# Performance work log

Hardware: AMD Instinct MI355X
Metric: run time of the kernel (lower is better)

The kernel has to match this reference:

```python
import jax, jax.numpy as jnp
import numpy as np

EMBED_DIM = 1024
NUM_HEADS = 16
HEAD_DIM = EMBED_DIM // NUM_HEADS
# Source divides by scale = head_dim**-0.5, i.e. multiplies logits by sqrt(head_dim).
INV_SCALE = float(HEAD_DIM) ** 0.5


def setup_inputs() -> dict:
    key = jax.random.key(0)
    ks = jax.random.split(key, 9)
    E = EMBED_DIM
    s = 1.0 / np.sqrt(E)
    x = jax.random.normal(ks[0], (2, 2048, E), dtype=jnp.float32)
    Wq = jax.random.uniform(ks[1], (E, E), jnp.float32, -s, s)
    bq = jax.random.uniform(ks[2], (E,), jnp.float32, -s, s)
    Wk = jax.random.uniform(ks[3], (E, E), jnp.float32, -s, s)
    bk = jax.random.uniform(ks[4], (E,), jnp.float32, -s, s)
    Wv = jax.random.uniform(ks[5], (E, E), jnp.float32, -s, s)
    bv = jax.random.uniform(ks[6], (E,), jnp.float32, -s, s)
    Wo = jax.random.uniform(ks[7], (E, E), jnp.float32, -s, s)
    bo = jax.random.uniform(ks[8], (E,), jnp.float32, -s, s)
    return {"x": x, "Wq": Wq, "bq": bq, "Wk": Wk, "bk": bk,
            "Wv": Wv, "bv": bv, "Wo": Wo, "bo": bo}


def reference(x, Wq, bq, Wk, bk, Wv, bv, Wo, bo):
    B, N, C = x.shape
    H, D = NUM_HEADS, HEAD_DIM
    # nn.Linear: y = x @ W.T + b
    q = (x @ Wq.T + bq).reshape(B, N, H, D).transpose(0, 2, 1, 3)  # [B,H,N,D]
    k = (x @ Wk.T + bk).reshape(B, N, H, D).transpose(0, 2, 1, 3)
    v = (x @ Wv.T + bv).reshape(B, N, H, D).transpose(0, 2, 1, 3)
    # Faithful to source: logits = QK^T / (head_dim**-0.5) = QK^T * sqrt(head_dim)
    logits = jnp.einsum('bhnd,bhmd->bhnm', q, k) * INV_SCALE  # [B,H,N,N]
    attn = jax.nn.softmax(logits, axis=-1)
    h = jnp.einsum('bhnm,bhmd->bhnd', attn, v)  # [B,H,N,D]
    concat_h = h.transpose(0, 2, 1, 3).reshape(B, N, C)
    return concat_h @ Wo.T + bo
```

## Files before the change

kernel.cpp:

```cpp
#include <hip/hip_runtime.h>
#include <math.h>

#define B_ 2
#define N_ 2048
#define E_ 1024
#define H_ 16
#define D_ 64

typedef unsigned short US;
typedef _Float16 h16x8 __attribute__((ext_vector_type(8)));
typedef _Float16 h16x4 __attribute__((ext_vector_type(4)));
typedef __fp16 fp16x2 __attribute__((ext_vector_type(2)));
typedef float f32x4 __attribute__((ext_vector_type(4)));
#define MFMA16F(a,b,c)  __builtin_amdgcn_mfma_f32_16x16x32_f16(a,b,c,0,0,0)
#define MFMA161(a,b,c)  __builtin_amdgcn_mfma_f32_16x16x16f16(a,b,c,0,0,0)
#define SCL  11.5415603828f

union HU { _Float16 h; US u; };
__device__ __forceinline__ US f2h(float f){ HU x; x.h = (_Float16)f; return x.u; }
__device__ __forceinline__ unsigned pkrtz(float a, float b){
  union { fp16x2 h; unsigned u; } x;
  x.h = __builtin_amdgcn_cvt_pkrtz(a, b);
  return x.u;
}

union U8 { US u[8]; uint4 v; };
union U4 { US u[4]; uint2 v; };
union UPA { unsigned u[2]; h16x4 h; };

__device__ __forceinline__ void glds16(const US* g, US* l){
  __builtin_amdgcn_global_load_lds(
    (const __attribute__((address_space(1))) unsigned int*)(const void*)g,
    (__attribute__((address_space(3))) unsigned int*)(void*)l, 16, 0, 0);
}

__global__ __launch_bounds__(256) void conv_all(
    const float* __restrict__ x,
    const float* __restrict__ w0, const float* __restrict__ w1,
    const float* __restrict__ w2, const float* __restrict__ w3,
    US* __restrict__ xh, US* __restrict__ Wall)
{
  const int id = blockIdx.x;
  const float* s; US* d; size_t off;
  if (id < 2048) { s = x; d = xh; off = (size_t)id*2048; }
  else {
    int j = id - 2048, wsel = j>>9;
    off = (size_t)(j&511)*2048;
    s = (wsel==0)?w0:(wsel==1)?w1:(wsel==2)?w2:w3;
    d = Wall + (size_t)wsel*1048576;
  }
  size_t i = off + (size_t)threadIdx.x*8;
  float f[8];
  *(float4*)&f[0] = *(const float4*)&s[i];
  *(float4*)&f[4] = *(const float4*)&s[i+4];
  U8 h;
  #pragma unroll
  for (int j=0;j<8;++j) h.u[j] = f2h(f[j]);
  *(uint4*)&d[i] = h.v;
}

__global__ __launch_bounds__(256,3) void qkv_gemm(
    const US* __restrict__ A, const US* __restrict__ Wall,
    const float* __restrict__ bq, const float* __restrict__ bk, const float* __restrict__ bv,
    US* __restrict__ Qf, US* __restrict__ Kf, US* __restrict__ Vtb)
{
  __shared__ __align__(16) US sA[128*32];
  __shared__ __align__(16) US sW[128*32];
  const int z = blockIdx.z;
  const US* W = Wall + (size_t)z*1048576;
  const float* bias = (z==0)?bq:(z==1)?bk:bv;

  const int t = threadIdx.x;
  const int w = t>>6, lane = t&63;
  const int q = lane>>4, c = lane&15;
  const int mq = (w>>1)*64, nq = (w&1)*64;
  const int gm0 = blockIdx.y*128, gn0 = blockIdx.x*128;
  const int r16 = lane>>2, seg = lane&3;

  f32x4 acc[4][4] = {};
  for (int kb = 0; kb < 1024; kb += 32) {
    #pragma unroll
    for (int p=0;p<2;++p){
      int rb = (w*2+p)*16;
      glds16(&A[(size_t)(gm0 + rb + r16)*1024 + kb + seg*8], &sA[rb*32]);
      glds16(&W[(size_t)(gn0 + rb + r16)*1024 + kb + seg*8], &sW[rb*32]);
    }
    __syncthreads();
    h16x8 af[4], wf[4];
    #pragma unroll
    for (int rt=0;rt<4;++rt) af[rt] = *(const h16x8*)&sA[(mq+rt*16+c)*32 + q*8];
    #pragma unroll
    for (int ct=0;ct<4;++ct) wf[ct] = *(const h16x8*)&sW[(nq+ct*16+c)*32 + q*8];
    #pragma unroll
    for (int rt=0;rt<4;++rt)
      #pragma unroll
      for (int ct=0;ct<4;++ct)
        acc[rt][ct] = MFMA16F(af[rt], wf[ct], acc[rt][ct]);
    __syncthreads();
  }
  #pragma unroll
  for (int rt=0;rt<4;++rt)
  #pragma unroll
  for (int ct=0;ct<4;++ct) {
    int col = gn0 + nq + ct*16 + c;
    float bv_ = bias[col];
    int rowb = gm0 + mq + rt*16 + q*4;
    int hh = col>>6, d = col & 63;
    if (z==2) {
      int b = rowb>>11, n = rowb & (N_-1);
      U4 pk;
      #pragma unroll
      for (int r=0;r<4;++r) pk.u[r] = f2h(acc[rt][ct][r] + bv_);
      *(uint2*)&Vtb[((size_t)(b*H_+hh)*D_ + d)*N_ + n] = pk.v;
    } else {
      US* dst = (z==0) ? Qf : Kf;
      #pragma unroll
      for (int r=0;r<4;++r) {
        int row = rowb + r;
        float v = acc[rt][ct][r] + bv_;
        if (z==0) v *= SCL;
        int b = row>>11, n = row & (N_-1);
        dst[((size_t)(b*H_+hh)*N_+n)*D_ + d] = f2h(v);
      }
    }
  }
}

__global__ __launch_bounds__(256,4) void o_gemm(
    const US* __restrict__ A, const US* __restrict__ W,
    const float* __restrict__ bias, float* __restrict__ out)
{
  __shared__ __align__(16) US sA[128*32];
  __shared__ __align__(16) US sW[64*32];
  const int t = threadIdx.x;
  const int w = t>>6, lane = t&63;
  const int q = lane>>4, c = lane&15;
  const int gm0 = blockIdx.y*128, gn0 = blockIdx.x*64;
  const int r16 = lane>>2, seg = lane&3;

  f32x4 acc[2][4] = {};
  for (int kb = 0; kb < 1024; kb += 32) {
    glds16(&A[(size_t)(gm0 + w*32      + r16)*1024 + kb + seg*8], &sA[(w*32)*32]);
    glds16(&A[(size_t)(gm0 + w*32 + 16 + r16)*1024 + kb + seg*8], &sA[(w*32+16)*32]);
    glds16(&W[(size_t)(gn0 + w*16      + r16)*1024 + kb + seg*8], &sW[(w*16)*32]);
    __syncthreads();
    h16x8 af0 = *(const h16x8*)&sA[(w*32+c)*32 + q*8];
    h16x8 af1 = *(const h16x8*)&sA[(w*32+16+c)*32 + q*8];
    #pragma unroll
    for (int ct=0; ct<4; ++ct){
      h16x8 wf = *(const h16x8*)&sW[(ct*16+c)*32 + q*8];
      acc[0][ct] = MFMA16F(af0, wf, acc[0][ct]);
      acc[1][ct] = MFMA16F(af1, wf, acc[1][ct]);
    }
    __syncthreads();
  }
  #pragma unroll
  for (int rt=0; rt<2; ++rt)
  #pragma unroll
  for (int ct=0; ct<4; ++ct) {
    int col = gn0 + ct*16 + c;
    float bv_ = bias[col];
    int rowb = gm0 + w*32 + rt*16 + q*4;
    #pragma unroll
    for (int r=0;r<4;++r)
      out[(size_t)(rowb+r)*1024 + col] = acc[rt][ct][r] + bv_;
  }
}

#define KSTR2 72
#define VSTR  136
__global__ __launch_bounds__(512,6) void attn(
    const US* __restrict__ Qf, const US* __restrict__ Kf, const US* __restrict__ Vt,
    US* __restrict__ Hout)
{
  __shared__ __align__(16) US sK [128*KSTR2];
  __shared__ __align__(16) US sVt[64*VSTR];
  const int t = threadIdx.x;
  const int w = t>>6, lane = t&63, q = lane>>4, c = lane&15;
  const int id = blockIdx.x;
  const int bh = ((id & 7) << 2) | ((id >> 3) & 3);
  const int n0 = (id >> 5) * 128;
  const US* Kp = Kf + (size_t)bh * (N_*D_);
  const US* Vp = Vt + (size_t)bh * (D_*N_);

  const size_t qoff = (size_t)bh*(N_*D_) + (size_t)(n0 + w*16 + c)*D_;
  h16x8 qb0 = *(const h16x8*)&Qf[qoff + q*8];
  h16x8 qb1 = *(const h16x8*)&Qf[qoff + 32 + q*8];
  h16x4 vones;
  #pragma unroll
  for (int j=0;j<4;++j) vones[j] = (_Float16)1.0f;

  float mi = -INFINITY;
  f32x4 o[5] = {};

  const int kr = t>>3, kc8 = (t&7)*8;
  const int vr = t>>4, vc8 = (t&15)*8;

  for (int mt=0; mt<16; ++mt) {
    const int m0 = mt*128;
    #pragma unroll
    for (int p=0;p<2;++p){
      int r = p*64 + kr;
      *(uint4*)&sK[r*KSTR2 + kc8] = *(const uint4*)&Kp[(size_t)(m0 + r)*D_ + kc8];
    }
    #pragma unroll
    for (int p=0;p<2;++p){
      int r = p*32 + vr;
      *(uint4*)&sVt[r*VSTR + vc8] = *(const uint4*)&Vp[(size_t)r*N_ + m0 + vc8];
    }
    __syncthreads();

    f32x4 s[8];
    __builtin_amdgcn_s_setprio(1);
    #pragma unroll
    for (int f=0; f<8; ++f){
      h16x8 k0 = *(const h16x8*)&sK[(f*16+c)*KSTR2 + q*8];
      h16x8 k1 = *(const h16x8*)&sK[(f*16+c)*KSTR2 + 32 + q*8];
      f32x4 sv = {};
      sv = MFMA16F(k0, qb0, sv);
      sv = MFMA16F(k1, qb1, sv);
      s[f] = sv;
    }
    __builtin_amdgcn_s_setprio(0);

    f32x4 vm = s[0];
    #pragma unroll
    for (int f=1; f<8; ++f){
      vm[0]=fmaxf(vm[0],s[f][0]); vm[1]=fmaxf(vm[1],s[f][1]);
      vm[2]=fmaxf(vm[2],s[f][2]); vm[3]=fmaxf(vm[3],s[f][3]);
    }
    float v = fmaxf(fmaxf(vm[0],vm[1]), fmaxf(vm[2],vm[3]));
    v = fmaxf(v, __shfl_xor(v, 16));
    v = fmaxf(v, __shfl_xor(v, 32));
    float mnew = fmaxf(mi, v);
    if (!__all(v <= mi)) {
      float alpha = exp2f(mi-mnew);
      float ar[4];
      #pragma unroll
      for (int r=0; r<4; ++r) ar[r] = __shfl(alpha, q*4+r);
      #pragma unroll
      for (int dt=0; dt<5; ++dt){
        o[dt][0]*=ar[0]; o[dt][1]*=ar[1]; o[dt][2]*=ar[2]; o[dt][3]*=ar[3];
      }
    }
    mi = mnew;
    #pragma unroll
    for (int f=0; f<8; ++f){
      float p0 = exp2f(s[f][0]-mnew);
      float p1 = exp2f(s[f][1]-mnew);
      float p2 = exp2f(s[f][2]-mnew);
      float p3 = exp2f(s[f][3]-mnew);
      UPA pa;
      pa.u[0] = pkrtz(p0, p1);
      pa.u[1] = pkrtz(p2, p3);
      h16x4 pah = pa.h;
      __builtin_amdgcn_s_setprio(1);
      #pragma unroll
      for (int dt=0; dt<4; ++dt){
        h16x4 vf = *(const h16x4*)&sVt[(dt*16+c)*VSTR + f*16 + q*4];
        o[dt] = MFMA161(pah, vf, o[dt]);
      }
      o[4] = MFMA161(pah, vones, o[4]);
      __builtin_amdgcn_s_setprio(0);
    }
    __syncthreads();
  }

  const int b = bh>>4, hh = bh&15;
  float ir[4];
  #pragma unroll
  for (int r=0; r<4; ++r) ir[r] = 1.0f / o[4][r];
  #pragma unroll
  for (int dt=0; dt<4; ++dt){
    #pragma unroll
    for (int r=0; r<4; ++r){
      int n = n0 + w*16 + q*4 + r;
      int d = dt*16 + c;
      Hout[((size_t)(b*N_+n)*H_+hh)*D_ + d] = f2h(o[dt][r] * ir[r]);
    }
  }
}

extern "C" void kernel_launch(void* const* d_in, const int* in_sizes, int n_in,
                              void* d_out, int out_size, void* d_ws, size_t ws_size,
                              hipStream_t stream)
{
  const float* x  = (const float*)d_in[0];
  const float* Wq = (const float*)d_in[1];
  const float* bq = (const float*)d_in[2];
  const float* Wk = (const float*)d_in[3];
  const float* bk = (const float*)d_in[4];
  const float* Wv = (const float*)d_in[5];
  const float* bv = (const float*)d_in[6];
  const float* Wo = (const float*)d_in[7];
  const float* bo = (const float*)d_in[8];
  US* ws  = (US*)d_ws;
  const size_t M1 = 1048576;
  US* xh   = ws;
  US* Wall = ws + 4*M1;
  US* Qf   = ws + 8*M1;
  US* Kf   = ws + 12*M1;
  US* Vtb  = ws + 16*M1;
  US* Hf   = ws + 20*M1;

  conv_all<<<4096, 256, 0, stream>>>(x, Wq, Wk, Wv, Wo, xh, Wall);
  qkv_gemm<<<dim3(8,32,3), 256, 0, stream>>>(xh, Wall, bq, bk, bv, Qf, Kf, Vtb);
  attn<<<512, 512, 0, stream>>>(Qf, Kf, Vtb, Hf);
  o_gemm<<<dim3(16,32), 256, 0, stream>>>(Hf, Wall + 3*M1, bo, (float*)d_out);
}
```

Before: 223.5 us.

## Double-buffer K/V tiles in attention with register prefetch of next tile

Makes the K and V shared-memory tiles double-buffered. The next tile's global loads are issued into registers before the QK^T and PV compute and written to the alternate buffer afterwards, so only one barrier per iteration remains. The goal is to hide global-memory latency behind MFMA work. In exchange, LDS use doubles, launch bounds drop from 6 to 4 blocks per CU, and the prefetch registers add register pressure.

```diff
diff --git a/kernel.cpp b/kernel.cpp
--- a/kernel.cpp
+++ b/kernel.cpp
@@ -169,12 +169,12 @@
 
 #define KSTR2 72
 #define VSTR  136
-__global__ __launch_bounds__(512,6) void attn(
+__global__ __launch_bounds__(512,4) void attn(
     const US* __restrict__ Qf, const US* __restrict__ Kf, const US* __restrict__ Vt,
     US* __restrict__ Hout)
 {
-  __shared__ __align__(16) US sK [128*KSTR2];
-  __shared__ __align__(16) US sVt[64*VSTR];
+  __shared__ __align__(16) US sK [2][128*KSTR2];
+  __shared__ __align__(16) US sVt[2][64*VSTR];
   const int t = threadIdx.x;
   const int w = t>>6, lane = t&63, q = lane>>4, c = lane&15;
   const int id = blockIdx.x;
@@ -196,26 +196,37 @@
   const int kr = t>>3, kc8 = (t&7)*8;
   const int vr = t>>4, vc8 = (t&15)*8;
 
+  #pragma unroll
+  for (int p=0;p<2;++p){
+    int r = p*64 + kr;
+    *(uint4*)&sK[0][r*KSTR2 + kc8] = *(const uint4*)&Kp[(size_t)r*D_ + kc8];
+  }
+  #pragma unroll
+  for (int p=0;p<2;++p){
+    int r = p*32 + vr;
+    *(uint4*)&sVt[0][r*VSTR + vc8] = *(const uint4*)&Vp[(size_t)r*N_ + vc8];
+  }
+  __syncthreads();
+
   for (int mt=0; mt<16; ++mt) {
-    const int m0 = mt*128;
-    #pragma unroll
-    for (int p=0;p<2;++p){
-      int r = p*64 + kr;
-      *(uint4*)&sK[r*KSTR2 + kc8] = *(const uint4*)&Kp[(size_t)(m0 + r)*D_ + kc8];
-    }
-    #pragma unroll
-    for (int p=0;p<2;++p){
-      int r = p*32 + vr;
-      *(uint4*)&sVt[r*VSTR + vc8] = *(const uint4*)&Vp[(size_t)r*N_ + m0 + vc8];
-    }
-    __syncthreads();
+    const int cur = mt&1;
+    uint4 kreg[2], vreg[2];
+    if (mt < 15){
+      const int m1 = (mt+1)*128;
+      #pragma unroll
+      for (int p=0;p<2;++p)
+        kreg[p] = *(const uint4*)&Kp[(size_t)(m1 + p*64 + kr)*D_ + kc8];
+      #pragma unroll
+      for (int p=0;p<2;++p)
+        vreg[p] = *(const uint4*)&Vp[(size_t)(p*32 + vr)*N_ + m1 + vc8];
+    }
 
     f32x4 s[8];
     __builtin_amdgcn_s_setprio(1);
     #pragma unroll
     for (int f=0; f<8; ++f){
-      h16x8 k0 = *(const h16x8*)&sK[(f*16+c)*KSTR2 + q*8];
-      h16x8 k1 = *(const h16x8*)&sK[(f*16+c)*KSTR2 + 32 + q*8];
+      h16x8 k0 = *(const h16x8*)&sK[cur][(f*16+c)*KSTR2 + q*8];
+      h16x8 k1 = *(const h16x8*)&sK[cur][(f*16+c)*KSTR2 + 32 + q*8];
       f32x4 sv = {};
       sv = MFMA16F(k0, qb0, sv);
       sv = MFMA16F(k1, qb1, sv);
@@ -257,11 +268,20 @@
       __builtin_amdgcn_s_setprio(1);
       #pragma unroll
       for (int dt=0; dt<4; ++dt){
-        h16x4 vf = *(const h16x4*)&sVt[(dt*16+c)*VSTR + f*16 + q*4];
+        h16x4 vf = *(const h16x4*)&sVt[cur][(dt*16+c)*VSTR + f*16 + q*4];
         o[dt] = MFMA161(pah, vf, o[dt]);
       }
       o[4] = MFMA161(pah, vones, o[4]);
       __builtin_amdgcn_s_setprio(0);
+    }
+
+    if (mt < 15){
+      #pragma unroll
+      for (int p=0;p<2;++p)
+        *(uint4*)&sK[cur^1][(p*64+kr)*KSTR2 + kc8] = kreg[p];
+      #pragma unroll
+      for (int p=0;p<2;++p)
+        *(uint4*)&sVt[cur^1][(p*32+vr)*VSTR + vc8] = vreg[p];
     }
     __syncthreads();
   }
```

Result: faster. 209.9 us (-6.1%).

## Double-buffer K/V tiles with direct global-to-LDS loads and software-pipelined QK

Applied to the files above, without the earlier changes.

Double-buffers the K and V^T tiles in shared memory and loads them with asynchronous global-to-LDS copies (glds16) into XOR-swizzled layouts instead of padded strides. The QK^T MFMAs for the next tile are issued alongside the PV MFMAs of the current tile, overlapping memory latency with compute. It also adds lazy max rescaling that only updates the running max when it grows by more than 8 in log2 space, and a tree-shaped max reduction. Shared memory use rises and the occupancy hint drops from 6 to 4 waves. The lazy rescale lets exponentials reach up to 2^8 before being rounded to fp16.

```diff
diff --git a/kernel.cpp b/kernel.cpp
--- a/kernel.cpp
+++ b/kernel.cpp
@@ -167,14 +167,12 @@
   }
 }
 
-#define KSTR2 72
-#define VSTR  136
-__global__ __launch_bounds__(512,6) void attn(
+__global__ __launch_bounds__(512,4) void attn(
     const US* __restrict__ Qf, const US* __restrict__ Kf, const US* __restrict__ Vt,
     US* __restrict__ Hout)
 {
-  __shared__ __align__(16) US sK [128*KSTR2];
-  __shared__ __align__(16) US sVt[64*VSTR];
+  __shared__ __align__(16) US sK [2][128*64];
+  __shared__ __align__(16) US sVt[2][64*128];
   const int t = threadIdx.x;
   const int w = t>>6, lane = t&63, q = lane>>4, c = lane&15;
   const int id = blockIdx.x;
@@ -193,48 +191,57 @@
   float mi = -INFINITY;
   f32x4 o[5] = {};
 
-  const int kr = t>>3, kc8 = (t&7)*8;
-  const int vr = t>>4, vc8 = (t&15)*8;
+  const int klr = lane>>3, klc = lane&7;
+  const int vlr = lane>>4, vlc = lane&15;
+
+  #define STAGE(MT, BUF)                                                              \
+    { const int m0_ = (MT)*128;                                                       \
+      _Pragma("unroll")                                                               \
+      for (int p=0;p<2;++p){                                                          \
+        int ch = 2*w + p;                                                             \
+        int row = ch*8 + klr;                                                         \
+        glds16(&Kp[(size_t)(m0_+row)*D_ + ((klc ^ (row&7))<<3)], &sK[BUF][ch<<9]);    \
+      }                                                                               \
+      _Pragma("unroll")                                                               \
+      for (int p=0;p<2;++p){                                                          \
+        int ch = 2*w + p;                                                             \
+        int row = ch*4 + vlr;                                                         \
+        glds16(&Vp[(size_t)row*N_ + m0_ + ((vlc ^ (row&15))<<3)], &sVt[BUF][ch<<9]);  \
+      }                                                                               \
+    }
+
+  STAGE(0, 0);
+  __syncthreads();
+  f32x4 s[8];
+  #pragma unroll
+  for (int f=0; f<8; ++f){
+    int r8 = (f*16+c)*64;
+    h16x8 k0 = *(const h16x8*)&sK[0][r8 + (( q      ^ (c&7))<<3)];
+    h16x8 k1 = *(const h16x8*)&sK[0][r8 + (((q+4)   ^ (c&7))<<3)];
+    f32x4 sv = {};
+    sv = MFMA16F(k0, qb0, sv);
+    sv = MFMA16F(k1, qb1, sv);
+    s[f] = sv;
+  }
 
   for (int mt=0; mt<16; ++mt) {
-    const int m0 = mt*128;
-    #pragma unroll
-    for (int p=0;p<2;++p){
-      int r = p*64 + kr;
-      *(uint4*)&sK[r*KSTR2 + kc8] = *(const uint4*)&Kp[(size_t)(m0 + r)*D_ + kc8];
-    }
-    #pragma unroll
-    for (int p=0;p<2;++p){
-      int r = p*32 + vr;
-      *(uint4*)&sVt[r*VSTR + vc8] = *(const uint4*)&Vp[(size_t)r*N_ + m0 + vc8];
-    }
-    __syncthreads();
-
-    f32x4 s[8];
-    __builtin_amdgcn_s_setprio(1);
-    #pragma unroll
-    for (int f=0; f<8; ++f){
-      h16x8 k0 = *(const h16x8*)&sK[(f*16+c)*KSTR2 + q*8];
-      h16x8 k1 = *(const h16x8*)&sK[(f*16+c)*KSTR2 + 32 + q*8];
-      f32x4 sv = {};
-      sv = MFMA16F(k0, qb0, sv);
-      sv = MFMA16F(k1, qb1, sv);
-      s[f] = sv;
-    }
-    __builtin_amdgcn_s_setprio(0);
-
-    f32x4 vm = s[0];
-    #pragma unroll
-    for (int f=1; f<8; ++f){
-      vm[0]=fmaxf(vm[0],s[f][0]); vm[1]=fmaxf(vm[1],s[f][1]);
-      vm[2]=fmaxf(vm[2],s[f][2]); vm[3]=fmaxf(vm[3],s[f][3]);
-    }
-    float v = fmaxf(fmaxf(vm[0],vm[1]), fmaxf(vm[2],vm[3]));
+    const int cur = mt&1;
+    if (mt < 15) STAGE(mt+1, cur^1);
+
+    f32x4 t1, t2;
+    #pragma unroll
+    for (int j=0;j<4;++j){
+      float a = fmaxf(fmaxf(s[0][j],s[1][j]),s[2][j]);
+      float b = fmaxf(fmaxf(s[3][j],s[4][j]),s[5][j]);
+      float d = fmaxf(fmaxf(s[6][j],s[7][j]),a);
+      t1[j] = fmaxf(b,d);
+    }
+    float v = fmaxf(fmaxf(t1[0],t1[1]), fmaxf(t1[2],t1[3]));
     v = fmaxf(v, __shfl_xor(v, 16));
     v = fmaxf(v, __shfl_xor(v, 32));
-    float mnew = fmaxf(mi, v);
-    if (!__all(v <= mi)) {
-      float alpha = exp2f(mi-mnew);
+    if (!__all(v <= mi + 8.0f)) {
+      float mnew = fmaxf(mi, v);
+      float alpha = exp2f(mi - mnew);
       float ar[4];
       #pragma unroll
       for (int r=0; r<4; ++r) ar[r] = __shfl(alpha, q*4+r);
@@ -242,29 +249,48 @@
       for (int dt=0; dt<5; ++dt){
         o[dt][0]*=ar[0]; o[dt][1]*=ar[1]; o[dt][2]*=ar[2]; o[dt][3]*=ar[3];
       }
-    }
-    mi = mnew;
+      mi = mnew;
+    }
+    UPA pa_[8];
     #pragma unroll
     for (int f=0; f<8; ++f){
-      float p0 = exp2f(s[f][0]-mnew);
-      float p1 = exp2f(s[f][1]-mnew);
-      float p2 = exp2f(s[f][2]-mnew);
-      float p3 = exp2f(s[f][3]-mnew);
-      UPA pa;
-      pa.u[0] = pkrtz(p0, p1);
-      pa.u[1] = pkrtz(p2, p3);
-      h16x4 pah = pa.h;
-      __builtin_amdgcn_s_setprio(1);
+      float p0 = exp2f(s[f][0]-mi);
+      float p1 = exp2f(s[f][1]-mi);
+      float p2 = exp2f(s[f][2]-mi);
+      float p3 = exp2f(s[f][3]-mi);
+      pa_[f].u[0] = pkrtz(p0, p1);
+      pa_[f].u[1] = pkrtz(p2, p3);
+    }
+
+    __syncthreads();
+
+    __builtin_amdgcn_s_setprio(1);
+    if (mt < 15){
+      #pragma unroll
+      for (int f=0; f<8; ++f){
+        int r8 = (f*16+c)*64;
+        h16x8 k0 = *(const h16x8*)&sK[cur^1][r8 + (( q    ^ (c&7))<<3)];
+        h16x8 k1 = *(const h16x8*)&sK[cur^1][r8 + (((q+4) ^ (c&7))<<3)];
+        f32x4 sv = {};
+        sv = MFMA16F(k0, qb0, sv);
+        sv = MFMA16F(k1, qb1, sv);
+        s[f] = sv;
+      }
+    }
+    #pragma unroll
+    for (int f=0; f<8; ++f){
+      h16x4 pah = pa_[f].h;
       #pragma unroll
       for (int dt=0; dt<4; ++dt){
-        h16x4 vf = *(const h16x4*)&sVt[(dt*16+c)*VSTR + f*16 + q*4];
+        h16x4 vf = *(const h16x4*)&sVt[cur][(dt*16+c)*128 + ((((f<<1)+(q>>1)) ^ c)<<3) + ((q&1)<<2)];
         o[dt] = MFMA161(pah, vf, o[dt]);
       }
       o[4] = MFMA161(pah, vones, o[4]);
-      __builtin_amdgcn_s_setprio(0);
-    }
-    __syncthreads();
-  }
+    }
+    __builtin_amdgcn_s_setprio(0);
+    __syncthreads();
+  }
+  #undef STAGE
 
   const int b = bh>>4, hh = bh&15;
   float ir[4];
```

Measured after the change: 218.7 us. 2.2% less time.
